# Optimization experiments

Hardware: AMD Instinct MI355X
Metric: run time of the kernel (lower is better)

Reference implementation:

```python
import jax, jax.numpy as jnp
import numpy as np

POOL = 7
IMG_H, IMG_W = 1024, 1024
CANONICAL = 224.0  # canonical box size used in the FPN level assignment


def _crop_and_resize(fm, boxes, ph, pw):
    """TF-style crop_and_resize (extrapolation_value=0).

    fm: [C, H, W] feature map; boxes: [N, 4] normalized (y1, x1, y2, x2).
    Returns [N, C, ph, pw] bilinearly sampled crops.
    """
    C, H, W = fm.shape
    y1, x1, y2, x2 = boxes[:, 0], boxes[:, 1], boxes[:, 2], boxes[:, 3]
    ty = jnp.arange(ph, dtype=boxes.dtype) / (ph - 1)  # [ph] in [0,1]
    tx = jnp.arange(pw, dtype=boxes.dtype) / (pw - 1)
    ys = (y1[:, None] + (y2 - y1)[:, None] * ty) * (H - 1)  # [N, ph] image coords
    xs = (x1[:, None] + (x2 - x1)[:, None] * tx) * (W - 1)  # [N, pw]
    yy = jnp.broadcast_to(ys[:, :, None], (ys.shape[0], ph, pw))  # [N, ph, pw]
    xx = jnp.broadcast_to(xs[:, None, :], (xs.shape[0], ph, pw))
    y0f = jnp.floor(yy)
    x0f = jnp.floor(xx)
    wy = yy - y0f
    wx = xx - x0f
    y0 = jnp.clip(y0f.astype(jnp.int32), 0, H - 1)
    y1i = jnp.clip(y0 + 1, 0, H - 1)
    x0 = jnp.clip(x0f.astype(jnp.int32), 0, W - 1)
    x1i = jnp.clip(x0 + 1, 0, W - 1)

    def g(yi, xi):
        return fm[:, yi, xi]  # [C, N, ph, pw]

    val = (g(y0, x0) * ((1 - wy) * (1 - wx))[None]
           + g(y0, x1i) * ((1 - wy) * wx)[None]
           + g(y1i, x0) * (wy * (1 - wx))[None]
           + g(y1i, x1i) * (wy * wx)[None])
    # extrapolation_value = 0 for samples outside the feature map
    inb = (yy >= 0) & (yy <= H - 1) & (xx >= 0) & (xx <= W - 1)
    val = jnp.where(inb[None], val, 0.0)
    return jnp.transpose(val, (1, 0, 2, 3))  # [N, C, ph, pw]


def setup_inputs() -> dict:
    key = jax.random.key(0)
    k1, k2, k3, k4, k5, k6, k7, k8 = jax.random.split(key, 8)
    N = 1000
    y1 = jax.random.uniform(k1, (N, 1)) * 0.7
    x1 = jax.random.uniform(k2, (N, 1)) * 0.7
    hh = jax.random.uniform(k3, (N, 1)) * 0.28 + 0.02
    ww = jax.random.uniform(k4, (N, 1)) * 0.28 + 0.02
    boxes = jnp.concatenate([y1, x1, y1 + hh, x1 + ww], axis=1)[None]  # [1,N,4]
    C = 256
    p2 = jax.random.normal(k5, (1, C, 256, 256), dtype=jnp.float32)
    p3 = jax.random.normal(k6, (1, C, 128, 128), dtype=jnp.float32)
    p4 = jax.random.normal(k7, (1, C, 64, 64), dtype=jnp.float32)
    p5 = jax.random.normal(k8, (1, C, 32, 32), dtype=jnp.float32)
    return {"boxes": boxes, "p2": p2, "p3": p3, "p4": p4, "p5": p5}


def reference(boxes, p2, p3, p4, p5):
    boxes = boxes[0]  # squeeze batch, [N,4]
    fms = [p2[0], p3[0], p4[0], p5[0]]  # each [C,H,W]
    y1, x1, y2, x2 = boxes[:, 0:1], boxes[:, 1:2], boxes[:, 2:3], boxes[:, 3:4]
    h = y2 - y1
    w = x2 - x1
    image_area = jnp.asarray(float(IMG_H * IMG_W), dtype=boxes.dtype)
    roi_level = 4 + jnp.log2(jnp.sqrt(h * w) / (CANONICAL / jnp.sqrt(image_area)))
    roi_level = jnp.clip(jnp.round(roi_level), 2, 5).astype(jnp.int32)[:, 0]  # [N]
    # Boxes are detached before cropping in the original (level_boxes.detach()).
    crop_boxes = jax.lax.stop_gradient(boxes)
    out = jnp.zeros((boxes.shape[0], fms[0].shape[0], POOL, POOL), dtype=boxes.dtype)
    for i, level in enumerate(range(2, 6)):
        crop = _crop_and_resize(fms[i], crop_boxes, POOL, POOL)
        sel = (roi_level == level)[:, None, None, None]
        out = out + jnp.where(sel, crop, 0.0)
    return out  # [N, C, POOL, POOL], original box order (sort restores order)
```

## Files before the change

### kernel.cpp

```cpp
#include <hip/hip_runtime.h>

#define POOL 7
#define NCH 256
#define OUT_PER_BOX (NCH * POOL * POOL)
#define PARTS 7
#define PART_SZ (OUT_PER_BOX / PARTS)
#define ITERS (PART_SZ / 256)
#define NXCD 8

__device__ __forceinline__ unsigned part1by1(unsigned x) {
    x &= 0x0000FFFFu;
    x = (x | (x << 8)) & 0x00FF00FFu;
    x = (x | (x << 4)) & 0x0F0F0F0Fu;
    x = (x | (x << 2)) & 0x33333333u;
    x = (x | (x << 1)) & 0x55555555u;
    return x;
}

__global__ __launch_bounds__(1024) void sort_boxes_kernel(
    const float* __restrict__ boxes, int* __restrict__ perm, int nbox)
{
    __shared__ unsigned s_key[1024];
    const int i = threadIdx.x;

    unsigned key = 0xFFFFFFFFu;
    if (i < nbox) {
        const float y1 = boxes[i * 4 + 0];
        const float x1 = boxes[i * 4 + 1];
        const float y2 = boxes[i * 4 + 2];
        const float x2 = boxes[i * 4 + 3];
        const float h = y2 - y1;
        const float w = x2 - x1;
        const float lvlf = 4.0f + log2f(sqrtf(h * w) * (1.0f / 0.21875f));
        int lvl = (int)rintf(lvlf);
        lvl = lvl < 2 ? 2 : (lvl > 5 ? 5 : lvl);

        const float cy = 0.5f * (y1 + y2);
        const float cx = 0.5f * (x1 + x2);
        unsigned qy = (unsigned)fminf(511.0f, fmaxf(0.0f, cy * 512.0f));
        unsigned qx = (unsigned)fminf(511.0f, fmaxf(0.0f, cx * 512.0f));
        const unsigned morton = (part1by1(qy) << 1) | part1by1(qx);

        key = ((unsigned)(lvl - 2) << 28) | (morton << 10) | (unsigned)i;
    }
    s_key[i] = key;
    __syncthreads();

    for (int k = 2; k <= 1024; k <<= 1) {
        for (int j = k >> 1; j > 0; j >>= 1) {
            const int p = i ^ j;
            if (p > i) {
                const unsigned a = s_key[i];
                const unsigned b = s_key[p];
                const bool up = ((i & k) == 0);
                if ((a > b) == up) { s_key[i] = b; s_key[p] = a; }
            }
            __syncthreads();
        }
    }

    if (i < nbox) perm[i] = (int)(s_key[i] & 1023u);
}

__global__ void identity_perm_kernel(int* __restrict__ perm, int nbox) {
    const int i = blockIdx.x * blockDim.x + threadIdx.x;
    if (i < nbox) perm[i] = i;
}

__global__ __launch_bounds__(256) void roi_align_kernel(
    const float* __restrict__ boxes,
    const float* __restrict__ p2,
    const float* __restrict__ p3,
    const float* __restrict__ p4,
    const float* __restrict__ p5,
    float* __restrict__ out,
    const int* __restrict__ perm,
    int nbox, int cpx)
{
    const int c    = blockIdx.x & (NXCD - 1);
    const int k    = blockIdx.x >> 3;
    const int l    = k / PARTS;
    const int part = k - l * PARTS;
    const int s    = c * cpx + l;
    if (s >= nbox) return;
    const int n = perm[s];
    const int tid = threadIdx.x;

    __shared__ int   s_y0[POOL], s_y1[POOL], s_xb[POOL], s_xcl[POOL];
    __shared__ float s_wy[POOL], s_wx[POOL], s_vy[POOL], s_vx[POOL];

    const float by1 = boxes[n * 4 + 0];
    const float bx1 = boxes[n * 4 + 1];
    const float by2 = boxes[n * 4 + 2];
    const float bx2 = boxes[n * 4 + 3];
    const float h = by2 - by1;
    const float w = bx2 - bx1;

    const float lvlf = 4.0f + log2f(sqrtf(h * w) / 0.21875f);
    int lvl = (int)rintf(lvlf);
    lvl = lvl < 2 ? 2 : (lvl > 5 ? 5 : lvl);

    const float* fm;
    int H;
    switch (lvl) {
        case 2:  fm = p2; H = 256; break;
        case 3:  fm = p3; H = 128; break;
        case 4:  fm = p4; H = 64;  break;
        default: fm = p5; H = 32;  break;
    }
    const float Hm1 = (float)(H - 1);

    if (tid < POOL) {
        const float t = (float)tid * (1.0f / 6.0f);

        const float yy  = (by1 + h * t) * Hm1;
        const float y0f = floorf(yy);
        int y0 = (int)y0f;
        y0 = min(H - 1, max(0, y0));
        s_y0[tid] = y0;
        s_y1[tid] = min(H - 1, y0 + 1);
        s_wy[tid] = yy - y0f;
        s_vy[tid] = (yy >= 0.0f && yy <= Hm1) ? 1.0f : 0.0f;

        const float xx  = (bx1 + w * t) * Hm1;
        const float x0f = floorf(xx);
        int x0 = (int)x0f;
        x0 = min(H - 1, max(0, x0));
        s_xb[tid]  = min(x0, H - 2);
        s_xcl[tid] = (x0 == H - 1) ? 1 : 0;
        s_wx[tid]  = xx - x0f;
        s_vx[tid]  = (xx >= 0.0f && xx <= Hm1) ? 1.0f : 0.0f;
    }
    __syncthreads();

    const size_t out_base = (size_t)n * OUT_PER_BOX + (size_t)part * PART_SZ;
    const int idx0 = part * PART_SZ + tid;
    const int HW = H * H;

    float2 q0[ITERS], q1[ITERS];
    #pragma unroll
    for (int i = 0; i < ITERS; ++i) {
        const int idx = idx0 + i * 256;
        const int cch = idx / 49;
        const int r   = idx - cch * 49;
        const int py  = r / 7;
        const int px  = r - py * 7;

        const float* fmc = fm + (size_t)cch * HW;
        const int xb = s_xb[px];
        q0[i] = *(const float2*)(fmc + s_y0[py] * H + xb);
        q1[i] = *(const float2*)(fmc + s_y1[py] * H + xb);
    }

    #pragma unroll
    for (int i = 0; i < ITERS; ++i) {
        const int idx = idx0 + i * 256;
        const int cch = idx / 49;
        const int r   = idx - cch * 49;
        const int py  = r / 7;
        const int px  = r - py * 7;

        const float wy = s_wy[py], wx = s_wx[px];
        const int   cl = s_xcl[px];

        const float v00 = cl ? q0[i].y : q0[i].x;
        const float v01 = q0[i].y;
        const float v10 = cl ? q1[i].y : q1[i].x;
        const float v11 = q1[i].y;

        const float r0 = v00 + wx * (v01 - v00);
        const float r1 = v10 + wx * (v11 - v10);
        float val = (r0 + wy * (r1 - r0)) * s_vy[py] * s_vx[px];

        out[out_base + (size_t)(i * 256 + tid)] = val;
    }
}

extern "C" void kernel_launch(void* const* d_in, const int* in_sizes, int n_in,
                              void* d_out, int out_size, void* d_ws, size_t ws_size,
                              hipStream_t stream) {
    const float* boxes = (const float*)d_in[0];
    const float* p2    = (const float*)d_in[1];
    const float* p3    = (const float*)d_in[2];
    const float* p4    = (const float*)d_in[3];
    const float* p5    = (const float*)d_in[4];
    float* out         = (float*)d_out;
    int*   perm        = (int*)d_ws;

    const int nbox = in_sizes[0] / 4;
    const int cpx  = (nbox + NXCD - 1) / NXCD;

    if (nbox <= 1024) {
        sort_boxes_kernel<<<1, 1024, 0, stream>>>(boxes, perm, nbox);
    } else {
        identity_perm_kernel<<<(nbox + 255) / 256, 256, 0, stream>>>(perm, nbox);
    }

    roi_align_kernel<<<NXCD * cpx * PARTS, 256, 0, stream>>>(
        boxes, p2, p3, p4, p5, out, perm, nbox, cpx);
}
```

Measured before the change: 184.8 us.

## Replace bitonic Morton sort with coarse binning and interleave box chunks across XCDs

Swaps the 1024-thread bitonic sort on level+Morton keys for a single-pass counting sort into 64 bins (level × 4x4 spatial grid), which removes the many barrier-separated sort stages. The main kernel's block-to-work mapping also changes. Instead of giving each XCD a contiguous slice of sorted boxes, it deals out chunks of 8 boxes × 7 parts round-robin across XCDs, so neighbouring boxes in the sorted order land on all XCDs at once. Coarser binning weakens spatial locality within a level, and the new mapping changes how feature-map data is shared in each XCD's L2.

```diff
diff --git a/kernel.cpp b/kernel.cpp
--- a/kernel.cpp
+++ b/kernel.cpp
@@ -7,23 +7,23 @@
 #define PART_SZ (OUT_PER_BOX / PARTS)
 #define ITERS (PART_SZ / 256)
 #define NXCD 8
+#define CHB 8
+#define CHU (CHB * PARTS)
+#define GRPU (NXCD * CHU)
 
-__device__ __forceinline__ unsigned part1by1(unsigned x) {
-    x &= 0x0000FFFFu;
-    x = (x | (x << 8)) & 0x00FF00FFu;
-    x = (x | (x << 4)) & 0x0F0F0F0Fu;
-    x = (x | (x << 2)) & 0x33333333u;
-    x = (x | (x << 1)) & 0x55555555u;
-    return x;
-}
+#define NBINS 64
 
-__global__ __launch_bounds__(1024) void sort_boxes_kernel(
+__global__ __launch_bounds__(1024) void bin_boxes_kernel(
     const float* __restrict__ boxes, int* __restrict__ perm, int nbox)
 {
-    __shared__ unsigned s_key[1024];
+    __shared__ int s_cnt[NBINS];
+    __shared__ int s_off[NBINS];
     const int i = threadIdx.x;
 
-    unsigned key = 0xFFFFFFFFu;
+    if (i < NBINS) s_cnt[i] = 0;
+    __syncthreads();
+
+    int bin = -1;
     if (i < nbox) {
         const float y1 = boxes[i * 4 + 0];
         const float x1 = boxes[i * 4 + 1];
@@ -37,29 +37,24 @@
 
         const float cy = 0.5f * (y1 + y2);
         const float cx = 0.5f * (x1 + x2);
-        unsigned qy = (unsigned)fminf(511.0f, fmaxf(0.0f, cy * 512.0f));
-        unsigned qx = (unsigned)fminf(511.0f, fmaxf(0.0f, cx * 512.0f));
-        const unsigned morton = (part1by1(qy) << 1) | part1by1(qx);
+        int qy = (int)(cy * 4.0f); qy = qy < 0 ? 0 : (qy > 3 ? 3 : qy);
+        int qx = (int)(cx * 4.0f); qx = qx < 0 ? 0 : (qx > 3 ? 3 : qx);
 
-        key = ((unsigned)(lvl - 2) << 28) | (morton << 10) | (unsigned)i;
+        bin = ((lvl - 2) << 4) | (qy << 2) | qx;
+        atomicAdd(&s_cnt[bin], 1);
     }
-    s_key[i] = key;
     __syncthreads();
 
-    for (int k = 2; k <= 1024; k <<= 1) {
-        for (int j = k >> 1; j > 0; j >>= 1) {
-            const int p = i ^ j;
-            if (p > i) {
-                const unsigned a = s_key[i];
-                const unsigned b = s_key[p];
-                const bool up = ((i & k) == 0);
-                if ((a > b) == up) { s_key[i] = b; s_key[p] = a; }
-            }
-            __syncthreads();
-        }
+    if (i == 0) {
+        int acc = 0;
+        for (int b = 0; b < NBINS; ++b) { s_off[b] = acc; acc += s_cnt[b]; }
     }
+    __syncthreads();
 
-    if (i < nbox) perm[i] = (int)(s_key[i] & 1023u);
+    if (i < nbox) {
+        const int pos = atomicAdd(&s_off[bin], 1);
+        perm[pos] = i;
+    }
 }
 
 __global__ void identity_perm_kernel(int* __restrict__ perm, int nbox) {
@@ -75,16 +70,18 @@
     const float* __restrict__ p5,
     float* __restrict__ out,
     const int* __restrict__ perm,
-    int nbox, int cpx)
+    int nbox, int total_u)
 {
-    const int c    = blockIdx.x & (NXCD - 1);
-    const int k    = blockIdx.x >> 3;
-    const int l    = k / PARTS;
-    const int part = k - l * PARTS;
-    const int s    = c * cpx + l;
-    if (s >= nbox) return;
-    const int n = perm[s];
-    const int tid = threadIdx.x;
+    const int xcd    = blockIdx.x & (NXCD - 1);
+    const int t      = blockIdx.x >> 3;
+    const int grp    = t / CHU;
+    const int within = t - grp * CHU;
+    const int u      = grp * GRPU + xcd * CHU + within;
+    if (u >= total_u) return;
+    const int s    = u / PARTS;
+    const int part = u - s * PARTS;
+    const int n    = perm[s];
+    const int tid  = threadIdx.x;
 
     __shared__ int   s_y0[POOL], s_y1[POOL], s_xb[POOL], s_xcl[POOL];
     __shared__ float s_wy[POOL], s_wx[POOL], s_vy[POOL], s_vx[POOL];
@@ -111,9 +108,9 @@
     const float Hm1 = (float)(H - 1);
 
     if (tid < POOL) {
-        const float t = (float)tid * (1.0f / 6.0f);
+        const float t7 = (float)tid * (1.0f / 6.0f);
 
-        const float yy  = (by1 + h * t) * Hm1;
+        const float yy  = (by1 + h * t7) * Hm1;
         const float y0f = floorf(yy);
         int y0 = (int)y0f;
         y0 = min(H - 1, max(0, y0));
@@ -122,7 +119,7 @@
         s_wy[tid] = yy - y0f;
         s_vy[tid] = (yy >= 0.0f && yy <= Hm1) ? 1.0f : 0.0f;
 
-        const float xx  = (bx1 + w * t) * Hm1;
+        const float xx  = (bx1 + w * t7) * Hm1;
         const float x0f = floorf(xx);
         int x0 = (int)x0f;
         x0 = min(H - 1, max(0, x0));
@@ -187,15 +184,16 @@
     float* out         = (float*)d_out;
     int*   perm        = (int*)d_ws;
 
-    const int nbox = in_sizes[0] / 4;
-    const int cpx  = (nbox + NXCD - 1) / NXCD;
+    const int nbox    = in_sizes[0] / 4;
+    const int total_u = nbox * PARTS;
+    const int grid    = ((total_u + GRPU - 1) / GRPU) * GRPU;
 
     if (nbox <= 1024) {
-        sort_boxes_kernel<<<1, 1024, 0, stream>>>(boxes, perm, nbox);
+        bin_boxes_kernel<<<1, 1024, 0, stream>>>(boxes, perm, nbox);
     } else {
         identity_perm_kernel<<<(nbox + 255) / 256, 256, 0, stream>>>(perm, nbox);
     }
 
-    roi_align_kernel<<<NXCD * cpx * PARTS, 256, 0, stream>>>(
-        boxes, p2, p3, p4, p5, out, perm, nbox, cpx);
+    roi_align_kernel<<<grid, 256, 0, stream>>>(
+        boxes, p2, p3, p4, p5, out, perm, nbox, total_u);
 }
```

After: 155.1 us. -16.0%, faster.
